# Kernel tuning notes

Measured on AMD Instinct MI355X. Metric: run time of the kernel, lower is better.

## Reference

```python
import jax, jax.numpy as jnp
import numpy as np

B, S, IN_DIM, D_MODEL, NUM_HEADS = 4, 2048, 1024, 1024, 16
HEAD_DIM = D_MODEL // NUM_HEADS
CAUSAL = True
NEG = -9000000000000000.0


def _xavier(key, shape):
    fan_out, fan_in = shape
    limit = (6.0 / (fan_in + fan_out)) ** 0.5
    return jax.random.uniform(key, shape, jnp.float32, -limit, limit)


def setup_inputs() -> dict:
    key = jax.random.key(0)
    ks = jax.random.split(key, 5)
    x = jax.random.normal(ks[0], (B, S, IN_DIM), jnp.float32)
    Wq = _xavier(ks[1], (D_MODEL, IN_DIM))
    Wk = _xavier(ks[2], (D_MODEL, IN_DIM))
    Wv = _xavier(ks[3], (D_MODEL, IN_DIM))
    Wo = _xavier(ks[4], (D_MODEL, D_MODEL))
    bq = jnp.zeros((D_MODEL,), jnp.float32)
    bk = jnp.zeros((D_MODEL,), jnp.float32)
    bv = jnp.zeros((D_MODEL,), jnp.float32)
    bo = jnp.zeros((D_MODEL,), jnp.float32)
    return {"x": x, "Wq": Wq, "bq": bq, "Wk": Wk, "bk": bk,
            "Wv": Wv, "bv": bv, "Wo": Wo, "bo": bo}


def reference(x, Wq, bq, Wk, bk, Wv, bv, Wo, bo):
    batch, seq, _ = x.shape
    # torch Linear: y = x @ W.T + b
    q = x @ Wq.T + bq
    k = x @ Wk.T + bk
    v = x @ Wv.T + bv
    # [B, S, H, Dh] -> [B, H, S, Dh]
    def split(t):
        return t.reshape(batch, seq, NUM_HEADS, HEAD_DIM).transpose(0, 2, 1, 3)
    q, k, v = split(q), split(k), split(v)
    scores = jnp.einsum('bhqd,bhkd->bhqk', q, k) / jnp.sqrt(jnp.float32(HEAD_DIM))
    if CAUSAL:
        mask = jnp.tril(jnp.ones((seq, seq), bool))
        scores = jnp.where(mask, scores, jnp.float32(NEG))
    attn = jax.nn.softmax(scores, axis=-1)
    out = jnp.einsum('bhqk,bhkd->bhqd', attn, v)
    out = out.transpose(0, 2, 1, 3).reshape(batch, seq, D_MODEL)
    return out @ Wo.T + bo
```

## Files before the change

kernel.cpp:

```cpp
#include <hip/hip_runtime.h>
#include <cstdint>
#include <cmath>

typedef unsigned short u16;
typedef __attribute__((ext_vector_type(4))) float f32x4;
typedef __attribute__((ext_vector_type(8))) short bf16x8;

#define D_MODEL 1024
#define SEQ     2048
#define BATCH   4
#define NHEAD   16
#define MTOT    (BATCH*SEQ)
#define NXE     ((size_t)MTOT * D_MODEL)

static_assert(sizeof(bf16x8) == 16, "frag size");

__device__ __forceinline__ float bf2f(u16 u) {
    union { uint32_t i; float f; } v; v.i = ((uint32_t)u) << 16; return v.f;
}
__device__ __forceinline__ u16 f2bf(float x) {
    union { float f; uint32_t i; } v; v.f = x;
    uint32_t r = (v.i + 0x7FFFu + ((v.i >> 16) & 1u)) >> 16;
    return (u16)r;
}
__device__ __forceinline__ u16 f2bf_trunc(float x) {
    union { float f; uint32_t i; } v; v.f = x;
    return (u16)(v.i >> 16);
}

typedef const __attribute__((address_space(1))) void* gptr_t;
typedef __attribute__((address_space(3))) void* sptr_t;
__device__ __forceinline__ void gload_lds16(const void* g, void* l) {
    __builtin_amdgcn_global_load_lds((gptr_t)g, (sptr_t)l, 16, 0, 0);
}

__global__ __launch_bounds__(256) void diag_write(float* __restrict__ out, float v) {
    size_t i = (size_t)blockIdx.x * 256 + threadIdx.x;
    for (; i < NXE; i += (size_t)gridDim.x * 256) out[i] = v;
}

__global__ void detect_dtype(const u16* __restrict__ x, int* __restrict__ flag) {
    __shared__ int cnt;
    if (threadIdx.x == 0) cnt = 0;
    __syncthreads();
    int c = 0;
#pragma unroll
    for (int k = 0; k < 16; ++k) {
        u16 e = x[2 * (threadIdx.x * 16 + k)];
        int ex = (e >> 7) & 0xFF;
        if (e == 0 || (ex >= 100 && ex <= 140)) ++c;
    }
    atomicAdd(&cnt, c);
    __syncthreads();
    if (threadIdx.x == 0) *flag = (cnt >= 3500) ? 1 : 0;
}

struct CvtArgs { const void* src[9]; u16* dst[9]; int n[9]; };

__global__ __launch_bounds__(256) void cvt_all(CvtArgs a, const int* __restrict__ flag) {
    const int seg = blockIdx.y;
    const int n = a.n[seg];
    const int i = (blockIdx.x * 256 + threadIdx.x) * 8;
    if (i >= n) return;
    u16* d = a.dst[seg] + i;
    if (*flag) {
        *(uint4*)d = *(const uint4*)((const u16*)a.src[seg] + i);
    } else {
        const float* s = (const float*)a.src[seg] + i;
        u16 tmp[8];
#pragma unroll
        for (int k = 0; k < 8; ++k) tmp[k] = f2bf(s[k]);
        *(uint4*)d = *(uint4*)tmp;
    }
}

template <typename OutT>
__device__ __forceinline__ void gemm_body(
    const u16* __restrict__ A, const u16* __restrict__ W,
    const u16* __restrict__ bias, OutT* __restrict__ C,
    int M, int N, int K)
{
    __shared__ __align__(16) u16 As[128 * 32];
    __shared__ __align__(16) u16 Bs[128 * 32];

    const int t    = threadIdx.x;
    const int wave = t >> 6;
    const int ln   = t & 15;
    const int qd   = (t >> 4) & 3;
    const int m0   = blockIdx.x * 128;
    const int n0   = blockIdx.y * 128;
    const int wm   = (wave >> 1) * 64;
    const int wn   = (wave & 1) * 64;

    const int srow = t >> 2;
    const int scol = (t & 3) * 8;
    const u16* gA = A + (size_t)(m0 + srow) * K + scol;
    const u16* gB = W + (size_t)(n0 + srow) * K + scol;
    u16* lA = &As[wave * 512];
    u16* lB = &Bs[wave * 512];

    f32x4 acc[4][4] = {};

    for (int k0 = 0; k0 < K; k0 += 32) {
        __syncthreads();
        gload_lds16(gA + k0,                   lA);
        gload_lds16(gA + (size_t)64 * K + k0,  lA + 2048);
        gload_lds16(gB + k0,                   lB);
        gload_lds16(gB + (size_t)64 * K + k0,  lB + 2048);
        __syncthreads();

        bf16x8 af[4], bfr[4];
#pragma unroll
        for (int i = 0; i < 4; ++i)
            af[i] = *(const bf16x8*)&As[(wm + i * 16 + ln) * 32 + qd * 8];
#pragma unroll
        for (int j = 0; j < 4; ++j)
            bfr[j] = *(const bf16x8*)&Bs[(wn + j * 16 + ln) * 32 + qd * 8];
#pragma unroll
        for (int i = 0; i < 4; ++i)
#pragma unroll
            for (int j = 0; j < 4; ++j)
                acc[i][j] = __builtin_amdgcn_mfma_f32_16x16x32_bf16(
                    af[i], bfr[j], acc[i][j], 0, 0, 0);
    }

    float bv[4];
#pragma unroll
    for (int j = 0; j < 4; ++j) bv[j] = bf2f(bias[n0 + wn + j * 16 + ln]);

#pragma unroll
    for (int i = 0; i < 4; ++i)
#pragma unroll
        for (int r = 0; r < 4; ++r) {
            int row = m0 + wm + i * 16 + qd * 4 + r;
            OutT* crow = C + (size_t)row * N + n0 + wn + ln;
#pragma unroll
            for (int j = 0; j < 4; ++j) {
                float v = acc[i][j][r] + bv[j];
                if constexpr (sizeof(OutT) == 2) crow[j * 16] = f2bf(v);
                else                             crow[j * 16] = v;
            }
        }
}

__global__ __launch_bounds__(256) void gemm_qkv(
    const u16* __restrict__ A,
    const u16* __restrict__ W0, const u16* __restrict__ W1, const u16* __restrict__ W2,
    const u16* __restrict__ b0, const u16* __restrict__ b1, const u16* __restrict__ b2,
    u16* __restrict__ C0, u16* __restrict__ C1, u16* __restrict__ C2,
    int M, int N, int K)
{
    const u16* W; const u16* bias; u16* C;
    if (blockIdx.z == 0)      { W = W0; bias = b0; C = C0; }
    else if (blockIdx.z == 1) { W = W1; bias = b1; C = C1; }
    else                      { W = W2; bias = b2; C = C2; }
    gemm_body<u16>(A, W, bias, C, M, N, K);
}

__global__ __launch_bounds__(256) void gemm_final_f32(
    const u16* __restrict__ A, const u16* __restrict__ W,
    const u16* __restrict__ bias, float* __restrict__ C, int M, int N, int K)
{
    gemm_body<float>(A, W, bias, C, M, N, K);
}

__global__ __launch_bounds__(64) void flash_attn(
    const u16* __restrict__ Qg, const u16* __restrict__ Kg,
    const u16* __restrict__ Vg, u16* __restrict__ Og)
{
    __shared__ __align__(16) u16 Vsh[64 * 64];
    __shared__ __align__(16) u16 Psh[32 * 64];

    const int lane = threadIdx.x;
    const int ln   = lane & 15;
    const int qd   = lane >> 4;
    const int psw  = (ln & 7) << 3;

    const int bh = blockIdx.y;
    const int qw = (63 - (int)blockIdx.x + bh) & 63;
    const int b  = bh >> 4;
    const int h  = bh & 15;
    const int h0 = h * 64;
    const size_t rowBase = (size_t)b * SEQ * D_MODEL;
    const int qw0 = qw * 32;
    const int ktMax = qw >> 1;

    const int vrL = lane >> 3;
    const int vcL = (lane & 7) * 8;

    bf16x8 qf[2][2];
#pragma unroll
    for (int i = 0; i < 2; ++i)
#pragma unroll
        for (int ks = 0; ks < 2; ++ks)
            qf[i][ks] = *(const bf16x8*)(Qg + rowBase
                + (size_t)(qw0 + i * 16 + ln) * D_MODEL + h0 + ks * 32 + qd * 8);

    float m_run[2], l_run[2];
#pragma unroll
    for (int i = 0; i < 2; ++i) { m_run[i] = -30000.0f; l_run[i] = 0.f; }
    f32x4 oacc[2][4] = {};

    for (int kt = 0; kt <= ktMax; ++kt) {
        __syncthreads();
        {
            const u16* vbase = Vg + rowBase
                + (size_t)(kt * 64 + vrL) * D_MODEL + h0;
#pragma unroll
            for (int p = 0; p < 8; ++p)
                gload_lds16(vbase + (size_t)(p * 8) * D_MODEL
                                  + (vcL ^ ((p & 3) << 4)),
                            &Vsh[p * 512]);
        }

        f32x4 sacc[4][2] = {};
#pragma unroll
        for (int ks = 0; ks < 2; ++ks) {
            bf16x8 kf[4];
#pragma unroll
            for (int j = 0; j < 4; ++j)
                kf[j] = *(const bf16x8*)(Kg + rowBase
                    + (size_t)(kt * 64 + j * 16 + ln) * D_MODEL + h0 + ks * 32 + qd * 8);
#pragma unroll
            for (int j = 0; j < 4; ++j)
#pragma unroll
                for (int i = 0; i < 2; ++i)
                    sacc[j][i] = __builtin_amdgcn_mfma_f32_16x16x32_bf16(
                        kf[j], qf[i][ks], sacc[j][i], 0, 0, 0);
        }

        if (kt == ktMax) {
#pragma unroll
            for (int j = 0; j < 4; ++j)
#pragma unroll
                for (int r = 0; r < 4; ++r) {
                    const int kpos = kt * 64 + j * 16 + qd * 4 + r;
#pragma unroll
                    for (int i = 0; i < 2; ++i) {
                        const int qpos = qw0 + i * 16 + ln;
                        float s = sacc[j][i][r] * 0.125f;
                        sacc[j][i][r] = (kpos > qpos) ? -30000.0f : s;
                    }
                }
        } else {
#pragma unroll
            for (int j = 0; j < 4; ++j)
#pragma unroll
                for (int i = 0; i < 2; ++i)
#pragma unroll
                    for (int r = 0; r < 4; ++r)
                        sacc[j][i][r] *= 0.125f;
        }

#pragma unroll
        for (int i = 0; i < 2; ++i) {
            float mx = sacc[0][i][0];
#pragma unroll
            for (int j = 0; j < 4; ++j)
#pragma unroll
                for (int r = 0; r < 4; ++r) mx = fmaxf(mx, sacc[j][i][r]);
            mx = fmaxf(mx, __shfl_xor(mx, 16));
            mx = fmaxf(mx, __shfl_xor(mx, 32));

            const float mo = m_run[i];
            const float mn = fmaxf(mo, mx);
            const float alpha = __expf(mo - mn);
            m_run[i] = mn;

            float rs = 0.f;
#pragma unroll
            for (int j = 0; j < 4; ++j) {
                u16 tp[4];
#pragma unroll
                for (int r = 0; r < 4; ++r) {
                    float p = __expf(sacc[j][i][r] - mn);
                    rs += p;
                    tp[r] = f2bf_trunc(p);
                }
                uint2 w;
                w.x = (uint32_t)tp[0] | ((uint32_t)tp[1] << 16);
                w.y = (uint32_t)tp[2] | ((uint32_t)tp[3] << 16);
                *(uint2*)&Psh[(i * 16 + ln) * 64 + ((j * 16 + qd * 4) ^ psw)] = w;
            }
            rs += __shfl_xor(rs, 16);
            rs += __shfl_xor(rs, 32);
            l_run[i] = l_run[i] * alpha + rs;

#pragma unroll
            for (int r = 0; r < 4; ++r) {
                const float ar = __shfl(alpha, qd * 4 + r);
#pragma unroll
                for (int j = 0; j < 4; ++j) oacc[i][j][r] *= ar;
            }
        }

        __syncthreads();

#pragma unroll
        for (int ks = 0; ks < 2; ++ks) {
            bf16x8 pa[2];
#pragma unroll
            for (int i = 0; i < 2; ++i)
                pa[i] = *(const bf16x8*)&Psh[(i * 16 + ln) * 64
                                             + ((ks * 32 + qd * 8) ^ psw)];
#pragma unroll
            for (int j = 0; j < 4; ++j) {
                const int vswz = qd << 4;
                bf16x8 vb;
#pragma unroll
                for (int e = 0; e < 8; ++e)
                    vb[e] = (short)Vsh[(ks * 32 + qd * 8 + e) * 64
                                       + ((j * 16 + ln) ^ vswz)];
#pragma unroll
                for (int i = 0; i < 2; ++i)
                    oacc[i][j] = __builtin_amdgcn_mfma_f32_16x16x32_bf16(
                        pa[i], vb, oacc[i][j], 0, 0, 0);
            }
        }
    }

#pragma unroll
    for (int i = 0; i < 2; ++i)
#pragma unroll
        for (int r = 0; r < 4; ++r) {
            const float lr = __shfl(l_run[i], qd * 4 + r);
            const float inv = 1.f / lr;
            const int qrow = qw0 + i * 16 + qd * 4 + r;
            u16* orow = Og + rowBase + (size_t)qrow * D_MODEL + h0 + ln;
#pragma unroll
            for (int j = 0; j < 4; ++j)
                orow[j * 16] = f2bf(oacc[i][j][r] * inv);
        }
}

static inline bool ranges_overlap(const void* a, size_t an, const void* b, size_t bn) {
    uintptr_t x0 = (uintptr_t)a, x1 = x0 + an;
    uintptr_t y0 = (uintptr_t)b, y1 = y0 + bn;
    return x0 < y1 && y0 < x1;
}

extern "C" void kernel_launch(void* const* d_in, const int* in_sizes, int n_in,
                              void* d_out, int out_size, void* d_ws, size_t ws_size,
                              hipStream_t stream)
{
    int e = 0;
    const int expect[9] = { 8388608, 1048576, 1024, 1048576, 1024,
                            1048576, 1024, 1048576, 1024 };
    if (n_in != 9) e = 59;
    if (!e) for (int i = 0; i < 9; ++i)
        if (in_sizes[i] != expect[i]) { e = 60 + i; break; }
    if (!e && out_size != (int)NXE) e = 53;
    if (!e && ranges_overlap(d_ws, ws_size, d_out, (size_t)out_size * 4)) e = 55;

    const size_t NX = NXE;
    const size_t NW = (size_t)D_MODEL * D_MODEL;
    const size_t NB = D_MODEL;

    const size_t need = (64 + 4 * NW + 4 * NB + 2 * NX) * 2;
    if (!e && ws_size < need) e = 50;
    if (e) { diag_write<<<2048, 256, 0, stream>>>((float*)d_out, ldexpf(1.0f, e)); return; }

    u16* ws   = (u16*)d_ws;
    int* flag = (int*)ws;
    u16* Wqb  = ws + 64;
    u16* Wkb  = Wqb + NW;
    u16* Wvb  = Wkb + NW;
    u16* Wob  = Wvb + NW;
    u16* bqb  = Wob + NW;
    u16* bkb  = bqb + NB;
    u16* bvb  = bkb + NB;
    u16* bob  = bvb + NB;
    u16* Kw   = bob + NB;
    u16* Vw   = Kw  + NX;

    u16* xb = (u16*)d_out;
    u16* Qw = xb + NX;
    u16* Aw = xb;
    float* Fout = (float*)Kw;

    detect_dtype<<<1, 256, 0, stream>>>((const u16*)d_in[0], flag);

    CvtArgs ca;
    const void* srcs[9] = { d_in[0], d_in[1], d_in[3], d_in[5], d_in[7],
                            d_in[2], d_in[4], d_in[6], d_in[8] };
    u16* dsts[9] = { xb, Wqb, Wkb, Wvb, Wob, bqb, bkb, bvb, bob };
    int  ns[9]   = { (int)NX, (int)NW, (int)NW, (int)NW, (int)NW,
                     (int)NB, (int)NB, (int)NB, (int)NB };
    for (int i = 0; i < 9; ++i) { ca.src[i] = srcs[i]; ca.dst[i] = dsts[i]; ca.n[i] = ns[i]; }
    cvt_all<<<dim3((unsigned)((NX + 2047) / 2048), 9), 256, 0, stream>>>(ca, flag);

    gemm_qkv<<<dim3(MTOT / 128, D_MODEL / 128, 3), 256, 0, stream>>>(
        xb, Wqb, Wkb, Wvb, bqb, bkb, bvb, Qw, Kw, Vw, MTOT, D_MODEL, D_MODEL);

    flash_attn<<<dim3(SEQ / 32, BATCH * NHEAD), 64, 0, stream>>>(Qw, Kw, Vw, Aw);

    gemm_final_f32<<<dim3(MTOT / 128, D_MODEL / 128), 256, 0, stream>>>(
        Aw, Wob, bob, Fout, MTOT, D_MODEL, D_MODEL);

    hipMemcpyAsync(d_out, Fout, NX * sizeof(float), hipMemcpyDeviceToDevice, stream);
}
```

Before: 349.7 us.

## Pre-transpose V per head and write final GEMM directly to output

Adds a transpose kernel that lays out V as [b*h, d, seq] so the attention kernel can load V tiles into LDS with contiguous rows and read B-fragments with one 16-byte vector load instead of eight scalar LDS reads. Buffers are rearranged so the attention output goes to the Vw workspace slot, which lets the final GEMM write straight into the fp32 output and removes the device-to-device copy. The cost is an extra kernel launch plus a read and write of V.

```diff
diff --git a/kernel.cpp b/kernel.cpp
--- a/kernel.cpp
+++ b/kernel.cpp
@@ -32,6 +32,12 @@
 typedef __attribute__((address_space(3))) void* sptr_t;
 __device__ __forceinline__ void gload_lds16(const void* g, void* l) {
     __builtin_amdgcn_global_load_lds((gptr_t)g, (sptr_t)l, 16, 0, 0);
+}
+
+__device__ __forceinline__ u16 u4get(const uint4& v, int e) {
+    const uint32_t w = ((e >> 1) == 0) ? v.x : ((e >> 1) == 1) ? v.y
+                     : ((e >> 1) == 2) ? v.z : v.w;
+    return (u16)((e & 1) ? (w >> 16) : (w & 0xFFFFu));
 }
 
 __global__ __launch_bounds__(256) void diag_write(float* __restrict__ out, float v) {
@@ -164,9 +170,37 @@
     gemm_body<float>(A, W, bias, C, M, N, K);
 }
 
+__global__ __launch_bounds__(256) void transpose_v(
+    const u16* __restrict__ V, u16* __restrict__ VT)
+{
+    __shared__ u16 T[64][72];
+    const int st = blockIdx.x;
+    const int bh = blockIdx.y;
+    const int b  = bh >> 4;
+    const int h  = bh & 15;
+    const int t  = threadIdx.x;
+
+    const int sr = t >> 2;
+    const int dc = (t & 3) * 16;
+    const u16* src = V + ((size_t)b * SEQ + st * 64 + sr) * D_MODEL + h * 64 + dc;
+    const uint4 a0 = *(const uint4*)src;
+    const uint4 a1 = *(const uint4*)(src + 8);
+#pragma unroll
+    for (int e = 0; e < 8; ++e) T[dc + e][sr]     = u4get(a0, e);
+#pragma unroll
+    for (int e = 0; e < 8; ++e) T[dc + 8 + e][sr] = u4get(a1, e);
+    __syncthreads();
+
+    const int d  = t >> 2;
+    const int sc = (t & 3) * 16;
+    u16* dst = VT + ((size_t)bh * 64 + d) * SEQ + st * 64 + sc;
+    *(uint4*)dst       = *(const uint4*)&T[d][sc];
+    *(uint4*)(dst + 8) = *(const uint4*)&T[d][sc + 8];
+}
+
 __global__ __launch_bounds__(64) void flash_attn(
     const u16* __restrict__ Qg, const u16* __restrict__ Kg,
-    const u16* __restrict__ Vg, u16* __restrict__ Og)
+    const u16* __restrict__ VTg, u16* __restrict__ Og)
 {
     __shared__ __align__(16) u16 Vsh[64 * 64];
     __shared__ __align__(16) u16 Psh[32 * 64];
@@ -185,8 +219,9 @@
     const int qw0 = qw * 32;
     const int ktMax = qw >> 1;
 
-    const int vrL = lane >> 3;
-    const int vcL = (lane & 7) * 8;
+    const int vdG = lane >> 3;
+    const int vsw = ((lane & 7) * 8) ^ (vdG << 3);
+    const u16* vtRow0 = VTg + ((size_t)(bh * 64 + vdG)) * SEQ + vsw;
 
     bf16x8 qf[2][2];
 #pragma unroll
@@ -204,13 +239,10 @@
     for (int kt = 0; kt <= ktMax; ++kt) {
         __syncthreads();
         {
-            const u16* vbase = Vg + rowBase
-                + (size_t)(kt * 64 + vrL) * D_MODEL + h0;
+            const u16* vbase = vtRow0 + kt * 64;
 #pragma unroll
             for (int p = 0; p < 8; ++p)
-                gload_lds16(vbase + (size_t)(p * 8) * D_MODEL
-                                  + (vcL ^ ((p & 3) << 4)),
-                            &Vsh[p * 512]);
+                gload_lds16(vbase + (size_t)(p * 8) * SEQ, &Vsh[p * 512]);
         }
 
         f32x4 sacc[4][2] = {};
@@ -305,12 +337,9 @@
                                              + ((ks * 32 + qd * 8) ^ psw)];
 #pragma unroll
             for (int j = 0; j < 4; ++j) {
-                const int vswz = qd << 4;
-                bf16x8 vb;
-#pragma unroll
-                for (int e = 0; e < 8; ++e)
-                    vb[e] = (short)Vsh[(ks * 32 + qd * 8 + e) * 64
-                                       + ((j * 16 + ln) ^ vswz)];
+                const int d = j * 16 + ln;
+                const bf16x8 vb = *(const bf16x8*)&Vsh[d * 64
+                    + ((ks * 32 + qd * 8) ^ ((ln & 7) << 3))];
 #pragma unroll
                 for (int i = 0; i < 2; ++i)
                     oacc[i][j] = __builtin_amdgcn_mfma_f32_16x16x32_bf16(
@@ -373,10 +402,10 @@
     u16* Kw   = bob + NB;
     u16* Vw   = Kw  + NX;
 
-    u16* xb = (u16*)d_out;
-    u16* Qw = xb + NX;
-    u16* Aw = xb;
-    float* Fout = (float*)Kw;
+    u16* xb  = (u16*)d_out;
+    u16* Qw  = xb + NX;
+    u16* VTw = xb;
+    u16* Ow  = Vw;
 
     detect_dtype<<<1, 256, 0, stream>>>((const u16*)d_in[0], flag);
 
@@ -392,10 +421,10 @@
     gemm_qkv<<<dim3(MTOT / 128, D_MODEL / 128, 3), 256, 0, stream>>>(
         xb, Wqb, Wkb, Wvb, bqb, bkb, bvb, Qw, Kw, Vw, MTOT, D_MODEL, D_MODEL);
 
-    flash_attn<<<dim3(SEQ / 32, BATCH * NHEAD), 64, 0, stream>>>(Qw, Kw, Vw, Aw);
+    transpose_v<<<dim3(SEQ / 64, BATCH * NHEAD), 256, 0, stream>>>(Vw, VTw);
+
+    flash_attn<<<dim3(SEQ / 32, BATCH * NHEAD), 64, 0, stream>>>(Qw, Kw, VTw, Ow);
 
     gemm_final_f32<<<dim3(MTOT / 128, D_MODEL / 128), 256, 0, stream>>>(
-        Aw, Wob, bob, Fout, MTOT, D_MODEL, D_MODEL);
-
-    hipMemcpyAsync(d_out, Fout, NX * sizeof(float), hipMemcpyDeviceToDevice, stream);
-}
+        Ow, Wob, bob, (float*)d_out, MTOT, D_MODEL, D_MODEL);
+}
```

Measured after the change: 338.6 us. 3.2% less time.
